# Performance work log

Hardware: AMD Instinct MI355X
Metric: run time of the kernel (lower is better)

## Reference

```python
import jax, jax.numpy as jnp
import numpy as np

EPS = 1e-6

def setup_inputs() -> dict:
    key = jax.random.key(0)
    k1, k2, k3 = jax.random.split(key, 3)
    B, N, D = 1, 2048, 1024
    x = jax.random.normal(k1, (B, N, D), dtype=jnp.float32)
    W_qvk = jax.random.normal(k2, (D, 3 * D), dtype=jnp.float32) * (D ** -0.5)
    b_qvk = jax.random.normal(k3, (3 * D,), dtype=jnp.float32) * 0.02
    return {"x": x, "W_qvk": W_qvk, "b_qvk": b_qvk, "head_num": 16}


def _forward(x, W_qvk, b_qvk, head_num):
    B, N, D = x.shape
    qvk = x @ W_qvk + b_qvk                       # (B, N, 3D)
    # torch.chunk order in source: q, v, k
    def to_heads(t):
        return t.reshape(B, N, head_num, D // head_num).transpose(0, 2, 1, 3)  # (B,h,N,e)
    q, v, k = (to_heads(t) for t in jnp.split(qvk, 3, axis=-1))
    e = q.shape[-1]
    # causal linear attention, bucket_size=1
    q = jax.nn.softmax(q, axis=-1) * (e ** -0.5)  # (B,h,N,e)
    k = jnp.exp(k)
    k_cumsum = jnp.cumsum(k, axis=2)              # (B,h,N,e)
    # per-position outer product k_i (x) v_i, then causal prefix-sum over N
    kv = jnp.einsum('bhnd,bhne->bhnde', k, v)     # (B,h,N,e,e)
    kv_cumsum = jnp.cumsum(kv, axis=2)            # (B,h,N,e,e)
    denom = jnp.einsum('bhnd,bhnd->bhn', q, k_cumsum + EPS)   # (B,h,N)
    out = jnp.einsum('bhnd,bhnde->bhne', q, kv_cumsum) / denom[..., None]
    # concat heads: (B,h,N,e) -> (B,N,D)
    return out.transpose(0, 2, 1, 3).reshape(B, N, D)


def reference(x, W_qvk, b_qvk, head_num):
    return _forward(x, W_qvk, b_qvk, head_num)
```

## Files before the change

kernel.cpp:

```cpp
#include <hip/hip_runtime.h>
#include <stdint.h>

#define NTOK 2048
#define NCH 32

typedef __attribute__((ext_vector_type(8))) short bf16x8;
typedef __attribute__((ext_vector_type(8))) unsigned short ushort8v;
typedef __attribute__((ext_vector_type(4))) float f32x4;

__device__ __forceinline__ unsigned short f2bf(float f) {
  unsigned u = __float_as_uint(f);
  u += 0x7fffu + ((u >> 16) & 1u);
  return (unsigned short)(u >> 16);
}
__device__ __forceinline__ float bf2f(unsigned short s) {
  return __uint_as_float(((unsigned)s) << 16);
}

__global__ __launch_bounds__(256) void k_prep_inputs(const float* __restrict__ x,
                                                     unsigned short* __restrict__ xb,
                                                     const float* __restrict__ W,
                                                     unsigned short* __restrict__ Wt) {
  int bid = blockIdx.x;
  if (bid < 2048) {
    int i = (bid * 256 + threadIdx.x) * 4;
    float4 v = *(const float4*)(x + i);
    ushort4 o = { f2bf(v.x), f2bf(v.y), f2bf(v.z), f2bf(v.w) };
    *(ushort4*)(xb + i) = o;
  } else {
    __shared__ float tile[32][33];
    int id = bid - 2048;
    int bx = id % 96, by = id / 96;
    int tx = threadIdx.x & 31, ty = threadIdx.x >> 5;
    int c0 = bx * 32;
    int r0 = by * 32;
#pragma unroll
    for (int j = 0; j < 32; j += 8)
      tile[ty + j][tx] = W[(size_t)(r0 + ty + j) * 3072 + c0 + tx];
    __syncthreads();
#pragma unroll
    for (int j = 0; j < 32; j += 8)
      Wt[(size_t)(c0 + ty + j) * 1024 + r0 + tx] = f2bf(tile[tx][ty + j]);
  }
}

__global__ __launch_bounds__(512) void k_gemm_fused(const unsigned short* __restrict__ xb,
                                                    const unsigned short* __restrict__ wt,
                                                    const float* __restrict__ bias,
                                                    unsigned short* __restrict__ qh,
                                                    unsigned short* __restrict__ kh,
                                                    unsigned short* __restrict__ kt,
                                                    unsigned short* __restrict__ vt) {
  __shared__ __align__(16) unsigned short As[2][128][64];
  __shared__ __align__(16) unsigned short Bs[2][128][64];
  const int t = threadIdx.x;
  const int lane = t & 63;
  const int wave = t >> 6;
  const int wr = wave >> 1;
  const int wc = wave & 1;
  const int rowBase = blockIdx.y * 128;
  const int colBase = blockIdx.x * 128;
  const int fr = lane & 15;
  const int khalf = lane >> 4;

  const int sr = t >> 3;
  const int ssl = (t & 7) ^ (sr & 7);
  const unsigned short* agB = xb + (size_t)(rowBase + sr) * 1024 + ssl * 8;
  const unsigned short* bgB = wt + (size_t)(colBase + sr) * 1024 + ssl * 8;
  char* laB = (char*)As + t * 16;
  char* lbB = (char*)Bs + t * 16;

#define STG(b, kt0) do {                                                                  \
    _Pragma("unroll")                                                                     \
    for (int i_ = 0; i_ < 2; ++i_) {                                                      \
      __builtin_amdgcn_global_load_lds(                                                   \
          (const __attribute__((address_space(1))) void*)(agB + (kt0) * 64 + i_ * 65536), \
          (__attribute__((address_space(3))) void*)(laB + (b) * 16384 + i_ * 8192), 16, 0, 0); \
      __builtin_amdgcn_global_load_lds(                                                   \
          (const __attribute__((address_space(1))) void*)(bgB + (kt0) * 64 + i_ * 65536), \
          (__attribute__((address_space(3))) void*)(lbB + (b) * 16384 + i_ * 8192), 16, 0, 0); \
    }                                                                                     \
  } while (0)

  f32x4 acc[2][4] = {};
  const int fs0 = khalf ^ (fr & 7);

#define FRAGS_MFMA(cur) do {                                                              \
    bf16x8 af[2][2], bff[4][2];                                                           \
    _Pragma("unroll")                                                                     \
    for (int m = 0; m < 2; ++m) {                                                         \
      const unsigned short* r = &As[cur][wr * 32 + m * 16 + fr][0];                       \
      af[m][0] = *(const bf16x8*)(r + fs0 * 8);                                           \
      af[m][1] = *(const bf16x8*)(r + (fs0 ^ 4) * 8);                                     \
    }                                                                                     \
    _Pragma("unroll")                                                                     \
    for (int n = 0; n < 4; ++n) {                                                         \
      const unsigned short* r = &Bs[cur][wc * 64 + n * 16 + fr][0];                       \
      bff[n][0] = *(const bf16x8*)(r + fs0 * 8);                                          \
      bff[n][1] = *(const bf16x8*)(r + (fs0 ^ 4) * 8);                                    \
    }                                                                                     \
    _Pragma("unroll")                                                                     \
    for (int m = 0; m < 2; ++m)                                                           \
      _Pragma("unroll")                                                                   \
      for (int n = 0; n < 4; ++n) {                                                       \
        acc[m][n] = __builtin_amdgcn_mfma_f32_16x16x32_bf16(af[m][0], bff[n][0], acc[m][n], 0, 0, 0); \
        acc[m][n] = __builtin_amdgcn_mfma_f32_16x16x32_bf16(af[m][1], bff[n][1], acc[m][n], 0, 0, 0); \
      }                                                                                   \
  } while (0)

  STG(0, 0);
  __syncthreads();
  int cur = 0;
#pragma unroll 1
  for (int ktile = 0; ktile < 15; ++ktile) {
    STG(cur ^ 1, ktile + 1);
    FRAGS_MFMA(cur);
    __syncthreads();
    cur ^= 1;
  }
  FRAGS_MFMA(cur);
#undef STG
#undef FRAGS_MFMA

  const int g = khalf;
  const int ocol = lane & 15;
  const int col0 = colBase + wc * 64;
  const int region = col0 >> 10;
  const int h = (col0 & 1023) >> 6;
  const int r0 = rowBase + wr * 32;
  const int cch = r0 >> 6;
  const int lbase = (wr & 1) * 32;
  float bv[4];
#pragma unroll
  for (int n = 0; n < 4; ++n) bv[n] = bias[col0 + 16 * n + ocol];

  if (region == 0) {
#pragma unroll
    for (int m = 0; m < 2; ++m) {
#pragma unroll
      for (int i = 0; i < 4; ++i) {
        float v[4];
#pragma unroll
        for (int n = 0; n < 4; ++n) v[n] = acc[m][n][i] + bv[n];
        float mx = fmaxf(fmaxf(v[0], v[1]), fmaxf(v[2], v[3]));
#pragma unroll
        for (int off = 1; off <= 8; off <<= 1) mx = fmaxf(mx, __shfl_xor(mx, off));
        float s = 0.f;
#pragma unroll
        for (int n = 0; n < 4; ++n) { v[n] = __expf(v[n] - mx); s += v[n]; }
#pragma unroll
        for (int off = 1; off <= 8; off <<= 1) s += __shfl_xor(s, off);
        float inv = 0.125f / s;
        int tok = r0 + 16 * m + 4 * g + i;
        unsigned short* qrow = qh + ((size_t)h * NTOK + tok) * 64;
#pragma unroll
        for (int n = 0; n < 4; ++n) qrow[16 * n + ocol] = f2bf(v[n] * inv);
      }
    }
  } else if (region == 1) {
    unsigned short* vb = vt + (size_t)(h * NCH + cch) * 4096;
#pragma unroll
    for (int m = 0; m < 2; ++m) {
      int tl = lbase + 16 * m + 4 * g;
#pragma unroll
      for (int n = 0; n < 4; ++n) {
        int e = 16 * n + ocol;
        ushort4 p = { f2bf(acc[m][n][0] + bv[n]), f2bf(acc[m][n][1] + bv[n]),
                      f2bf(acc[m][n][2] + bv[n]), f2bf(acc[m][n][3] + bv[n]) };
        *(ushort4*)&vb[(size_t)e * 64 + tl] = p;
      }
    }
  } else {
    unsigned short* kb = kt + (size_t)(h * NCH + cch) * 4096;
#pragma unroll
    for (int m = 0; m < 2; ++m) {
      int tl = lbase + 16 * m + 4 * g;
#pragma unroll
      for (int n = 0; n < 4; ++n) {
        int e = 16 * n + ocol;
        float kv[4];
#pragma unroll
        for (int i = 0; i < 4; ++i) kv[i] = __expf(acc[m][n][i] + bv[n]);
        ushort4 p = { f2bf(kv[0]), f2bf(kv[1]), f2bf(kv[2]), f2bf(kv[3]) };
        *(ushort4*)&kb[(size_t)e * 64 + tl] = p;
#pragma unroll
        for (int i = 0; i < 4; ++i)
          kh[((size_t)h * NTOK + r0 + 16 * m + 4 * g + i) * 64 + e] = p[i];
      }
    }
  }
}

__global__ __launch_bounds__(256) void k_chunk_sums(const unsigned short* __restrict__ kt,
                                                    const unsigned short* __restrict__ vt,
                                                    float* __restrict__ Sc,
                                                    float* __restrict__ zc) {
  int h = blockIdx.x >> 5, c = blockIdx.x & 31;
  __shared__ __align__(16) unsigned short Kt[64][72], Vt[64][72];
  int t = threadIdx.x, lane = t & 63, w = t >> 6;
  int fr = lane & 15, g = lane >> 4, fko = g * 8;
  const unsigned short* kg = kt + (size_t)(h * NCH + c) * 4096;
  const unsigned short* vg = vt + (size_t)(h * NCH + c) * 4096;
  for (int s = t; s < 512; s += 256) {
    int r = s >> 3, c8 = (s & 7) * 8;
    *(ushort8v*)&Kt[r][c8] = *(const ushort8v*)&kg[r * 64 + c8];
    *(ushort8v*)&Vt[r][c8] = *(const ushort8v*)&vg[r * 64 + c8];
  }
  __syncthreads();
  bf16x8 ka[2];
#pragma unroll
  for (int ks = 0; ks < 2; ++ks) ka[ks] = *(const bf16x8*)&Kt[16 * w + fr][32 * ks + fko];
  f32x4 s4[4] = {};
#pragma unroll
  for (int nb = 0; nb < 4; ++nb)
#pragma unroll
    for (int ks = 0; ks < 2; ++ks) {
      bf16x8 vf = *(const bf16x8*)&Vt[16 * nb + fr][32 * ks + fko];
      s4[nb] = __builtin_amdgcn_mfma_f32_16x16x32_bf16(ka[ks], vf, s4[nb], 0, 0, 0);
    }
  float* so = Sc + (size_t)(h * NCH + c) * 4096;
#pragma unroll
  for (int nb = 0; nb < 4; ++nb) {
    float4 o = { s4[nb][0], s4[nb][1], s4[nb][2], s4[nb][3] };
    *(float4*)&so[(size_t)(16 * nb + fr) * 64 + 16 * w + 4 * g] = o;
  }
  if (w == 0) {
    float z = 0.f;
#pragma unroll
    for (int j = 0; j < 8; ++j) {
      bf16x8 kv = *(const bf16x8*)&Kt[lane][j * 8];
#pragma unroll
      for (int e = 0; e < 8; ++e) z += bf2f((unsigned short)kv[e]);
    }
    zc[(size_t)(h * NCH + c) * 64 + lane] = z;
  }
}

__global__ __launch_bounds__(256) void k_scan(const float* __restrict__ Sc,
                                              unsigned short* __restrict__ Sp,
                                              const float* __restrict__ zc,
                                              float* __restrict__ zp) {
  int b = blockIdx.x;
  if (b < 256) {
    int tg = b * 256 + threadIdx.x;
    int h = tg >> 12, e = tg & 4095;
    float run = 0.f;
    for (int c = 0; c < NCH; ++c) {
      size_t idx = (size_t)(h * NCH + c) * 4096 + e;
      float v = Sc[idx];
      Sp[idx] = f2bf(run);
      run += v;
    }
  } else {
#pragma unroll
    for (int j = 0; j < 4; ++j) {
      int s = threadIdx.x + j * 256;
      int h = s >> 6, d = s & 63;
      float run = 0.f;
      for (int c = 0; c < NCH; ++c) {
        size_t idx = (size_t)(h * NCH + c) * 64 + d;
        zp[idx] = run;
        run += zc[idx];
      }
    }
  }
}

__global__ __launch_bounds__(256) void k_attn(const unsigned short* __restrict__ qh,
                                              const unsigned short* __restrict__ kh,
                                              const unsigned short* __restrict__ vt,
                                              const unsigned short* __restrict__ Sp,
                                              const float* __restrict__ zp,
                                              float* __restrict__ out) {
  int h = blockIdx.x >> 5, c = blockIdx.x & 31;
  __shared__ __align__(16) unsigned short Qs[64][72], Ks[64][72], Vts[64][72], Sts[64][72], Ams[64][72];
  __shared__ float zs[64], denom[64];
  int t = threadIdx.x, lane = t & 63, w = t >> 6;
  int fr = lane & 15, g = lane >> 4, fko = g * 8;
  const unsigned short* qg = qh + ((size_t)h * NTOK + c * 64) * 64;
  const unsigned short* kg = kh + ((size_t)h * NTOK + c * 64) * 64;
  const unsigned short* vg = vt + (size_t)(h * NCH + c) * 4096;
  const unsigned short* sg = Sp + (size_t)(h * NCH + c) * 4096;
  for (int s = t; s < 512; s += 256) {
    int r = s >> 3, c8 = (s & 7) * 8;
    *(ushort8v*)&Qs[r][c8]  = *(const ushort8v*)&qg[r * 64 + c8];
    *(ushort8v*)&Ks[r][c8]  = *(const ushort8v*)&kg[r * 64 + c8];
    *(ushort8v*)&Vts[r][c8] = *(const ushort8v*)&vg[r * 64 + c8];
    *(ushort8v*)&Sts[r][c8] = *(const ushort8v*)&sg[r * 64 + c8];
  }
  if (t < 64) zs[t] = zp[(size_t)(h * NCH + c) * 64 + t];
  __syncthreads();

  bf16x8 qa[2];
#pragma unroll
  for (int ks = 0; ks < 2; ++ks) qa[ks] = *(const bf16x8*)&Qs[16 * w + fr][32 * ks + fko];
  f32x4 a1[4] = {};
#pragma unroll
  for (int mb = 0; mb < 4; ++mb)
#pragma unroll
    for (int ks = 0; ks < 2; ++ks) {
      bf16x8 kf = *(const bf16x8*)&Ks[16 * mb + fr][32 * ks + fko];
      a1[mb] = __builtin_amdgcn_mfma_f32_16x16x32_bf16(qa[ks], kf, a1[mb], 0, 0, 0);
    }
#pragma unroll
  for (int i = 0; i < 4; ++i) {
    int n = 16 * w + 4 * g + i;
    float rs = 0.f;
#pragma unroll
    for (int j = 0; j < 4; ++j) rs += bf2f(Qs[n][fr * 4 + j]) * zs[fr * 4 + j];
#pragma unroll
    for (int mb = 0; mb < 4; ++mb) {
      int m = 16 * mb + fr;
      float v = (m <= n) ? a1[mb][i] : 0.f;
      a1[mb][i] = v;
      rs += v;
      Ams[n][16 * mb + fr] = f2bf(v);
    }
#pragma unroll
    for (int off = 1; off <= 8; off <<= 1) rs += __shfl_xor(rs, off);
    if (fr == 0) denom[n] = rs + 1.25e-7f;
  }
  __syncthreads();

  bf16x8 xa[4];
#pragma unroll
  for (int ks = 0; ks < 2; ++ks) {
    xa[ks]     = *(const bf16x8*)&Vts[16 * w + fr][32 * ks + fko];
    xa[2 + ks] = *(const bf16x8*)&Sts[16 * w + fr][32 * ks + fko];
  }
  f32x4 o4[4] = {};
#pragma unroll
  for (int nb = 0; nb < 4; ++nb)
#pragma unroll
    for (int ks = 0; ks < 2; ++ks) {
      bf16x8 afr = *(const bf16x8*)&Ams[16 * nb + fr][32 * ks + fko];
      o4[nb] = __builtin_amdgcn_mfma_f32_16x16x32_bf16(xa[ks], afr, o4[nb], 0, 0, 0);
      bf16x8 qfr = *(const bf16x8*)&Qs[16 * nb + fr][32 * ks + fko];
      o4[nb] = __builtin_amdgcn_mfma_f32_16x16x32_bf16(xa[2 + ks], qfr, o4[nb], 0, 0, 0);
    }
#pragma unroll
  for (int nb = 0; nb < 4; ++nb) {
    int n = 16 * nb + fr;
    float dv = denom[n];
    float4 res = { o4[nb][0] / dv, o4[nb][1] / dv, o4[nb][2] / dv, o4[nb][3] / dv };
    *(float4*)&out[(size_t)(c * 64 + n) * 1024 + h * 64 + 16 * w + 4 * g] = res;
  }
}

extern "C" void kernel_launch(void* const* d_in, const int* in_sizes, int n_in,
                              void* d_out, int out_size, void* d_ws, size_t ws_size,
                              hipStream_t stream) {
  (void)in_sizes; (void)n_in; (void)out_size; (void)ws_size;
  const float* x = (const float*)d_in[0];
  const float* W = (const float*)d_in[1];
  const float* b = (const float*)d_in[2];
  char* ws = (char*)d_ws;

  const size_t MB = 1024 * 1024;
  unsigned short* xb = (unsigned short*)(ws + 0);
  unsigned short* Wt = (unsigned short*)(ws + 4 * MB);
  unsigned short* qh = (unsigned short*)(ws + 10 * MB);
  unsigned short* kh = (unsigned short*)(ws + 14 * MB);
  unsigned short* kt = (unsigned short*)(ws + 18 * MB);
  unsigned short* vt = (unsigned short*)(ws + 22 * MB);
  float*          Sc = (float*)(ws + 26 * MB);
  unsigned short* Sp = (unsigned short*)(ws + 34 * MB);
  float*          zc = (float*)(ws + 38 * MB);
  float*          zp = (float*)(ws + 38 * MB + 131072);

  k_prep_inputs<<<dim3(5120), dim3(256), 0, stream>>>(x, xb, W, Wt);
  k_gemm_fused<<<dim3(24, 16), dim3(512), 0, stream>>>(xb, Wt, b, qh, kh, kt, vt);
  k_chunk_sums<<<dim3(512), dim3(256), 0, stream>>>(kt, vt, Sc, zc);
  k_scan<<<dim3(257), dim3(256), 0, stream>>>(Sc, Sp, zc, zp);
  k_attn<<<dim3(512), dim3(256), 0, stream>>>(qh, kh, vt, Sp, zp, (float*)d_out);
}
```

Measured before the change: 49.72 us.

## Triple-buffer GEMM with BK=32 and store chunk sums in bf16

The fused QKV GEMM moves from a double-buffered BK=64 swizzled LDS pipeline to a triple-buffered BK=32 pipeline. It uses explicit vmcnt waits, a single barrier per iteration and setprio around the MFMAs, and a launch_bounds occupancy hint is added. The aim is to overlap global-to-LDS loads with MFMA work and cut the number of syncs. The XOR swizzle is dropped, which may bring LDS bank conflicts. Separately, per-chunk KV sums are written in bf16 instead of fp32 to halve scan traffic, at some cost in precision.

```diff
diff --git a/kernel.cpp b/kernel.cpp
--- a/kernel.cpp
+++ b/kernel.cpp
@@ -44,15 +44,15 @@
   }
 }
 
-__global__ __launch_bounds__(512) void k_gemm_fused(const unsigned short* __restrict__ xb,
-                                                    const unsigned short* __restrict__ wt,
-                                                    const float* __restrict__ bias,
-                                                    unsigned short* __restrict__ qh,
-                                                    unsigned short* __restrict__ kh,
-                                                    unsigned short* __restrict__ kt,
-                                                    unsigned short* __restrict__ vt) {
-  __shared__ __align__(16) unsigned short As[2][128][64];
-  __shared__ __align__(16) unsigned short Bs[2][128][64];
+__global__ __launch_bounds__(512, 4) void k_gemm_fused(const unsigned short* __restrict__ xb,
+                                                       const unsigned short* __restrict__ wt,
+                                                       const float* __restrict__ bias,
+                                                       unsigned short* __restrict__ qh,
+                                                       unsigned short* __restrict__ kh,
+                                                       unsigned short* __restrict__ kt,
+                                                       unsigned short* __restrict__ vt) {
+  __shared__ __align__(16) unsigned short As[3][128][32];
+  __shared__ __align__(16) unsigned short Bs[3][128][32];
   const int t = threadIdx.x;
   const int lane = t & 63;
   const int wave = t >> 6;
@@ -63,66 +63,52 @@
   const int fr = lane & 15;
   const int khalf = lane >> 4;
 
-  const int sr = t >> 3;
-  const int ssl = (t & 7) ^ (sr & 7);
-  const unsigned short* agB = xb + (size_t)(rowBase + sr) * 1024 + ssl * 8;
-  const unsigned short* bgB = wt + (size_t)(colBase + sr) * 1024 + ssl * 8;
-  char* laB = (char*)As + t * 16;
-  char* lbB = (char*)Bs + t * 16;
-
-#define STG(b, kt0) do {                                                                  \
-    _Pragma("unroll")                                                                     \
-    for (int i_ = 0; i_ < 2; ++i_) {                                                      \
-      __builtin_amdgcn_global_load_lds(                                                   \
-          (const __attribute__((address_space(1))) void*)(agB + (kt0) * 64 + i_ * 65536), \
-          (__attribute__((address_space(3))) void*)(laB + (b) * 16384 + i_ * 8192), 16, 0, 0); \
-      __builtin_amdgcn_global_load_lds(                                                   \
-          (const __attribute__((address_space(1))) void*)(bgB + (kt0) * 64 + i_ * 65536), \
-          (__attribute__((address_space(3))) void*)(lbB + (b) * 16384 + i_ * 8192), 16, 0, 0); \
-    }                                                                                     \
+  const int srow = t >> 2;
+  const int sslot = t & 3;
+  const unsigned short* gA = xb + (size_t)(rowBase + srow) * 1024 + sslot * 8;
+  const unsigned short* gB = wt + (size_t)(colBase + srow) * 1024 + sslot * 8;
+  char* lA = (char*)As + t * 16;
+  char* lB = (char*)Bs + t * 16;
+
+#define STG(buf, kt0) do {                                                                \
+    __builtin_amdgcn_global_load_lds(                                                     \
+        (const __attribute__((address_space(1))) void*)(gA + (kt0) * 32),                 \
+        (__attribute__((address_space(3))) void*)(lA + (buf) * 8192), 16, 0, 0);          \
+    __builtin_amdgcn_global_load_lds(                                                     \
+        (const __attribute__((address_space(1))) void*)(gB + (kt0) * 32),                 \
+        (__attribute__((address_space(3))) void*)(lB + (buf) * 8192), 16, 0, 0);          \
   } while (0)
 
   f32x4 acc[2][4] = {};
-  const int fs0 = khalf ^ (fr & 7);
-
-#define FRAGS_MFMA(cur) do {                                                              \
-    bf16x8 af[2][2], bff[4][2];                                                           \
-    _Pragma("unroll")                                                                     \
-    for (int m = 0; m < 2; ++m) {                                                         \
-      const unsigned short* r = &As[cur][wr * 32 + m * 16 + fr][0];                       \
-      af[m][0] = *(const bf16x8*)(r + fs0 * 8);                                           \
-      af[m][1] = *(const bf16x8*)(r + (fs0 ^ 4) * 8);                                     \
-    }                                                                                     \
-    _Pragma("unroll")                                                                     \
-    for (int n = 0; n < 4; ++n) {                                                         \
-      const unsigned short* r = &Bs[cur][wc * 64 + n * 16 + fr][0];                       \
-      bff[n][0] = *(const bf16x8*)(r + fs0 * 8);                                          \
-      bff[n][1] = *(const bf16x8*)(r + (fs0 ^ 4) * 8);                                    \
-    }                                                                                     \
-    _Pragma("unroll")                                                                     \
-    for (int m = 0; m < 2; ++m)                                                           \
-      _Pragma("unroll")                                                                   \
-      for (int n = 0; n < 4; ++n) {                                                       \
-        acc[m][n] = __builtin_amdgcn_mfma_f32_16x16x32_bf16(af[m][0], bff[n][0], acc[m][n], 0, 0, 0); \
-        acc[m][n] = __builtin_amdgcn_mfma_f32_16x16x32_bf16(af[m][1], bff[n][1], acc[m][n], 0, 0, 0); \
-      }                                                                                   \
-  } while (0)
 
   STG(0, 0);
-  __syncthreads();
-  int cur = 0;
+  STG(1, 1);
 #pragma unroll 1
-  for (int ktile = 0; ktile < 15; ++ktile) {
-    STG(cur ^ 1, ktile + 1);
-    FRAGS_MFMA(cur);
-    __syncthreads();
-    cur ^= 1;
-  }
-  FRAGS_MFMA(cur);
+  for (int ktile = 0; ktile < 32; ++ktile) {
+    const int cur = ktile % 3;
+    if (ktile < 31) { asm volatile("s_waitcnt vmcnt(2)" ::: "memory"); }
+    else            { asm volatile("s_waitcnt vmcnt(0)" ::: "memory"); }
+    __builtin_amdgcn_s_barrier();
+    __builtin_amdgcn_sched_barrier(0);
+    if (ktile < 30) STG((ktile + 2) % 3, ktile + 2);
+    bf16x8 af[2], bff[4];
+#pragma unroll
+    for (int m = 0; m < 2; ++m)
+      af[m] = *(const bf16x8*)&As[cur][wr * 32 + m * 16 + fr][khalf * 8];
+#pragma unroll
+    for (int n = 0; n < 4; ++n)
+      bff[n] = *(const bf16x8*)&Bs[cur][wc * 64 + n * 16 + fr][khalf * 8];
+    __builtin_amdgcn_s_setprio(1);
+#pragma unroll
+    for (int m = 0; m < 2; ++m)
+#pragma unroll
+      for (int n = 0; n < 4; ++n)
+        acc[m][n] = __builtin_amdgcn_mfma_f32_16x16x32_bf16(af[m], bff[n], acc[m][n], 0, 0, 0);
+    __builtin_amdgcn_s_setprio(0);
+  }
 #undef STG
-#undef FRAGS_MFMA
-
-  const int g = khalf;
+
+  const int g2 = khalf;
   const int ocol = lane & 15;
   const int col0 = colBase + wc * 64;
   const int region = col0 >> 10;
@@ -151,7 +137,7 @@
 #pragma unroll
         for (int off = 1; off <= 8; off <<= 1) s += __shfl_xor(s, off);
         float inv = 0.125f / s;
-        int tok = r0 + 16 * m + 4 * g + i;
+        int tok = r0 + 16 * m + 4 * g2 + i;
         unsigned short* qrow = qh + ((size_t)h * NTOK + tok) * 64;
 #pragma unroll
         for (int n = 0; n < 4; ++n) qrow[16 * n + ocol] = f2bf(v[n] * inv);
@@ -161,7 +147,7 @@
     unsigned short* vb = vt + (size_t)(h * NCH + cch) * 4096;
 #pragma unroll
     for (int m = 0; m < 2; ++m) {
-      int tl = lbase + 16 * m + 4 * g;
+      int tl = lbase + 16 * m + 4 * g2;
 #pragma unroll
       for (int n = 0; n < 4; ++n) {
         int e = 16 * n + ocol;
@@ -174,7 +160,7 @@
     unsigned short* kb = kt + (size_t)(h * NCH + cch) * 4096;
 #pragma unroll
     for (int m = 0; m < 2; ++m) {
-      int tl = lbase + 16 * m + 4 * g;
+      int tl = lbase + 16 * m + 4 * g2;
 #pragma unroll
       for (int n = 0; n < 4; ++n) {
         int e = 16 * n + ocol;
@@ -185,7 +171,7 @@
         *(ushort4*)&kb[(size_t)e * 64 + tl] = p;
 #pragma unroll
         for (int i = 0; i < 4; ++i)
-          kh[((size_t)h * NTOK + r0 + 16 * m + 4 * g + i) * 64 + e] = p[i];
+          kh[((size_t)h * NTOK + r0 + 16 * m + 4 * g2 + i) * 64 + e] = p[i];
       }
     }
   }
@@ -193,7 +179,7 @@
 
 __global__ __launch_bounds__(256) void k_chunk_sums(const unsigned short* __restrict__ kt,
                                                     const unsigned short* __restrict__ vt,
-                                                    float* __restrict__ Sc,
+                                                    unsigned short* __restrict__ Sc,
                                                     float* __restrict__ zc) {
   int h = blockIdx.x >> 5, c = blockIdx.x & 31;
   __shared__ __align__(16) unsigned short Kt[64][72], Vt[64][72];
@@ -218,11 +204,11 @@
       bf16x8 vf = *(const bf16x8*)&Vt[16 * nb + fr][32 * ks + fko];
       s4[nb] = __builtin_amdgcn_mfma_f32_16x16x32_bf16(ka[ks], vf, s4[nb], 0, 0, 0);
     }
-  float* so = Sc + (size_t)(h * NCH + c) * 4096;
+  unsigned short* so = Sc + (size_t)(h * NCH + c) * 4096;
 #pragma unroll
   for (int nb = 0; nb < 4; ++nb) {
-    float4 o = { s4[nb][0], s4[nb][1], s4[nb][2], s4[nb][3] };
-    *(float4*)&so[(size_t)(16 * nb + fr) * 64 + 16 * w + 4 * g] = o;
+    ushort4 o = { f2bf(s4[nb][0]), f2bf(s4[nb][1]), f2bf(s4[nb][2]), f2bf(s4[nb][3]) };
+    *(ushort4*)&so[(size_t)(16 * nb + fr) * 64 + 16 * w + 4 * g] = o;
   }
   if (w == 0) {
     float z = 0.f;
@@ -236,7 +222,7 @@
   }
 }
 
-__global__ __launch_bounds__(256) void k_scan(const float* __restrict__ Sc,
+__global__ __launch_bounds__(256) void k_scan(const unsigned short* __restrict__ Sc,
                                               unsigned short* __restrict__ Sp,
                                               const float* __restrict__ zc,
                                               float* __restrict__ zp) {
@@ -247,7 +233,7 @@
     float run = 0.f;
     for (int c = 0; c < NCH; ++c) {
       size_t idx = (size_t)(h * NCH + c) * 4096 + e;
-      float v = Sc[idx];
+      float v = bf2f(Sc[idx]);
       Sp[idx] = f2bf(run);
       run += v;
     }
@@ -363,10 +349,10 @@
   unsigned short* kh = (unsigned short*)(ws + 14 * MB);
   unsigned short* kt = (unsigned short*)(ws + 18 * MB);
   unsigned short* vt = (unsigned short*)(ws + 22 * MB);
-  float*          Sc = (float*)(ws + 26 * MB);
-  unsigned short* Sp = (unsigned short*)(ws + 34 * MB);
-  float*          zc = (float*)(ws + 38 * MB);
-  float*          zp = (float*)(ws + 38 * MB + 131072);
+  unsigned short* Sc = (unsigned short*)(ws + 26 * MB);
+  unsigned short* Sp = (unsigned short*)(ws + 30 * MB);
+  float*          zc = (float*)(ws + 34 * MB);
+  float*          zp = (float*)(ws + 34 * MB + 131072);
 
   k_prep_inputs<<<dim3(5120), dim3(256), 0, stream>>>(x, xb, W, Wt);
   k_gemm_fused<<<dim3(24, 16), dim3(512), 0, stream>>>(xb, Wt, b, qh, kh, kt, vt);
```

Measured after the change: 55.33 us. +11.3%, slower.
